# Performance work log

Hardware: AMD Instinct MI355X
Metric: run time of the kernel (lower is better)

The kernel has to match this reference:

```python
import jax, jax.numpy as jnp
import numpy as np

EPS = 1e-13 + 1e-14  # matches torch: sqrt(sum(x^2)) + 1e-13 + 1e-14


def l2norm(x, dim=1):
    norm = jnp.sqrt(jnp.sum(x * x, axis=dim, keepdims=True)) + EPS
    return x / norm


def setup_inputs() -> dict:
    key = jax.random.key(0)
    k1, k2 = jax.random.split(key)
    N, D = 65536, 512
    s = jax.random.normal(k1, (N, D), dtype=jnp.float32)
    im = jax.random.normal(k2, (N, D), dtype=jnp.float32)
    return {"s": s, "im": im, "temp": 1000}


def reference(s, im, temp):
    # cosine_sim(s, im) followed by taking only the diagonal of the N x N
    # similarity matrix; diag(A) == diag(A.T), so the two directional losses
    # are identical and their average equals -sum(diag).
    sn = l2norm(s)   # [N, D]
    imn = l2norm(im)  # [N, D]
    diag = jnp.sum(sn * imn, axis=1)  # row-wise cosine similarity, [N]
    loss = -jnp.sum(diag)
    return loss
```

## Files before the change

kernel.cpp:

```cpp
#include <hip/hip_runtime.h>


#define EPSV 1.1e-13f

__global__ void zero_out_kernel(float* out) {
    out[0] = 0.0f;
}

__global__ __launch_bounds__(256, 4) void cosdiag_kernel(
        const float4* __restrict__ s,
        const float4* __restrict__ im,
        float* __restrict__ out,
        int nrows) {
    const int lane  = threadIdx.x & 63;
    const int wave  = threadIdx.x >> 6;
    const int wpb   = blockDim.x >> 6;
    const int gwave = blockIdx.x * wpb + wave;
    const int nwav  = gridDim.x * wpb;

    float acc = 0.0f;

    for (int row = gwave; row < nrows; row += nwav) {
        const float4* __restrict__ srow = s  + (size_t)row * 128;
        const float4* __restrict__ irow = im + (size_t)row * 128;
        float4 s0 = srow[lane];
        float4 s1 = srow[lane + 64];
        float4 i0 = irow[lane];
        float4 i1 = irow[lane + 64];

        float ss = s0.x*s0.x + s0.y*s0.y + s0.z*s0.z + s0.w*s0.w
                 + s1.x*s1.x + s1.y*s1.y + s1.z*s1.z + s1.w*s1.w;
        float ii = i0.x*i0.x + i0.y*i0.y + i0.z*i0.z + i0.w*i0.w
                 + i1.x*i1.x + i1.y*i1.y + i1.z*i1.z + i1.w*i1.w;
        float dt = s0.x*i0.x + s0.y*i0.y + s0.z*i0.z + s0.w*i0.w
                 + s1.x*i1.x + s1.y*i1.y + s1.z*i1.z + s1.w*i1.w;

        #pragma unroll
        for (int off = 32; off > 0; off >>= 1) {
            ss += __shfl_xor(ss, off);
            ii += __shfl_xor(ii, off);
            dt += __shfl_xor(dt, off);
        }

        if (lane == 0) {
            acc += dt / ((sqrtf(ss) + EPSV) * (sqrtf(ii) + EPSV));
        }
    }

    __shared__ float part[8];
    if (lane == 0) part[wave] = acc;
    __syncthreads();
    if (threadIdx.x == 0) {
        float bs = 0.0f;
        for (int w = 0; w < wpb; ++w) bs += part[w];
        atomicAdd(out, -bs);
    }
}

extern "C" void kernel_launch(void* const* d_in, const int* in_sizes, int n_in,
                              void* d_out, int out_size, void* d_ws, size_t ws_size,
                              hipStream_t stream) {
    const float* s  = (const float*)d_in[0];
    const float* im = (const float*)d_in[1];
    float* out = (float*)d_out;

    const int D = 512;
    const int nrows = in_sizes[0] / D;

    zero_out_kernel<<<1, 1, 0, stream>>>(out);

    const int block = 256;
    const int rows_per_block = block / 64;
    int grid = (nrows + rows_per_block - 1) / rows_per_block;
    if (grid > 2048) grid = 2048;

    cosdiag_kernel<<<grid, block, 0, stream>>>(
        (const float4*)s, (const float4*)im, out, nrows);
}
```

Baseline: 276.2 us.

## Map eight-lane groups to rows with unrolled loads and no grid-stride loop

New measurement: 277.3 us. About the same (+0.4%).

```diff
diff --git a/kernel.cpp b/kernel.cpp
--- a/kernel.cpp
+++ b/kernel.cpp
@@ -7,53 +7,56 @@
     out[0] = 0.0f;
 }
 
-__global__ __launch_bounds__(256, 4) void cosdiag_kernel(
+__global__ __launch_bounds__(256) void cosdiag_kernel(
         const float4* __restrict__ s,
         const float4* __restrict__ im,
         float* __restrict__ out,
         int nrows) {
-    const int lane  = threadIdx.x & 63;
-    const int wave  = threadIdx.x >> 6;
-    const int wpb   = blockDim.x >> 6;
-    const int gwave = blockIdx.x * wpb + wave;
-    const int nwav  = gridDim.x * wpb;
+    const int tid   = threadIdx.x;
+    const int lane  = tid & 63;
+    const int wave  = tid >> 6;
+    const int gwave = blockIdx.x * 4 + wave;
+    const int oct   = lane & 7;
+    const int lrow  = lane >> 3;
+    const int row   = gwave * 8 + lrow;
 
-    float acc = 0.0f;
+    float ss = 0.0f, ii = 0.0f, dt = 0.0f;
 
-    for (int row = gwave; row < nrows; row += nwav) {
-        const float4* __restrict__ srow = s  + (size_t)row * 128;
-        const float4* __restrict__ irow = im + (size_t)row * 128;
-        float4 s0 = srow[lane];
-        float4 s1 = srow[lane + 64];
-        float4 i0 = irow[lane];
-        float4 i1 = irow[lane + 64];
-
-        float ss = s0.x*s0.x + s0.y*s0.y + s0.z*s0.z + s0.w*s0.w
-                 + s1.x*s1.x + s1.y*s1.y + s1.z*s1.z + s1.w*s1.w;
-        float ii = i0.x*i0.x + i0.y*i0.y + i0.z*i0.z + i0.w*i0.w
-                 + i1.x*i1.x + i1.y*i1.y + i1.z*i1.z + i1.w*i1.w;
-        float dt = s0.x*i0.x + s0.y*i0.y + s0.z*i0.z + s0.w*i0.w
-                 + s1.x*i1.x + s1.y*i1.y + s1.z*i1.z + s1.w*i1.w;
+    if (row < nrows) {
+        const float4* __restrict__ srow = s  + (size_t)row * 128 + oct;
+        const float4* __restrict__ irow = im + (size_t)row * 128 + oct;
 
         #pragma unroll
-        for (int off = 32; off > 0; off >>= 1) {
-            ss += __shfl_xor(ss, off);
-            ii += __shfl_xor(ii, off);
-            dt += __shfl_xor(dt, off);
-        }
-
-        if (lane == 0) {
-            acc += dt / ((sqrtf(ss) + EPSV) * (sqrtf(ii) + EPSV));
+        for (int j = 0; j < 16; ++j) {
+            float4 a = srow[(size_t)j * 8];
+            float4 b = irow[(size_t)j * 8];
+            ss += a.x*a.x + a.y*a.y + a.z*a.z + a.w*a.w;
+            ii += b.x*b.x + b.y*b.y + b.z*b.z + b.w*b.w;
+            dt += a.x*b.x + a.y*b.y + a.z*b.z + a.w*b.w;
         }
     }
 
-    __shared__ float part[8];
-    if (lane == 0) part[wave] = acc;
+    #pragma unroll
+    for (int off = 1; off <= 4; off <<= 1) {
+        ss += __shfl_xor(ss, off);
+        ii += __shfl_xor(ii, off);
+        dt += __shfl_xor(dt, off);
+    }
+
+    float contrib = (oct == 0 && row < nrows)
+                  ? dt / ((sqrtf(ss) + EPSV) * (sqrtf(ii) + EPSV))
+                  : 0.0f;
+
+    #pragma unroll
+    for (int off = 8; off <= 32; off <<= 1) {
+        contrib += __shfl_xor(contrib, off);
+    }
+
+    __shared__ float part[4];
+    if (lane == 0) part[wave] = contrib;
     __syncthreads();
-    if (threadIdx.x == 0) {
-        float bs = 0.0f;
-        for (int w = 0; w < wpb; ++w) bs += part[w];
-        atomicAdd(out, -bs);
+    if (tid == 0) {
+        atomicAdd(out, -(part[0] + part[1] + part[2] + part[3]));
     }
 }
 
@@ -69,11 +72,9 @@
 
     zero_out_kernel<<<1, 1, 0, stream>>>(out);
 
-    const int block = 256;
-    const int rows_per_block = block / 64;
+    const int rows_per_block = 32;
     int grid = (nrows + rows_per_block - 1) / rows_per_block;
-    if (grid > 2048) grid = 2048;
 
-    cosdiag_kernel<<<grid, block, 0, stream>>>(
+    cosdiag_kernel<<<grid, 256, 0, stream>>>(
         (const float4*)s, (const float4*)im, out, nrows);
 }
```
